# Optimization experiments

Measured on AMD Instinct MI355X. Metric: run time of the kernel, lower is better.

Reference implementation:

```python
import jax, jax.numpy as jnp
import numpy as np

H = 2048   # hidden_size
V = 50257  # output_size (vocab)


def setup_inputs() -> dict:
    key = jax.random.key(0)
    ks = jax.random.split(key, 8)
    s = 1.0 / np.sqrt(H)
    return {
        "word":   jax.random.normal(ks[0], (H,), dtype=jnp.float32),
        "hidden": jax.random.normal(ks[1], (1, 1, H), dtype=jnp.float32),
        "w_ih":   jax.random.uniform(ks[2], (3 * H, H), jnp.float32, -s, s),
        "w_hh":   jax.random.uniform(ks[3], (3 * H, H), jnp.float32, -s, s),
        "b_ih":   jax.random.uniform(ks[4], (3 * H,), jnp.float32, -s, s),
        "b_hh":   jax.random.uniform(ks[5], (3 * H,), jnp.float32, -s, s),
        "lin_w":  jax.random.uniform(ks[6], (V, H), jnp.float32, -s, s),
        "lin_b":  jax.random.uniform(ks[7], (V,), jnp.float32, -s, s),
    }


def reference(word, hidden, w_ih, w_hh, b_ih, b_hh, lin_w, lin_b):
    h0 = hidden.reshape(-1)                      # (H,)
    gi = w_ih @ word + b_ih                      # (3H,) input gates
    gh = w_hh @ h0 + b_hh                        # (3H,) hidden gates
    i_r, i_z, i_n = gi[:H], gi[H:2 * H], gi[2 * H:]
    h_r, h_z, h_n = gh[:H], gh[H:2 * H], gh[2 * H:]
    r = jax.nn.sigmoid(i_r + h_r)
    z = jax.nn.sigmoid(i_z + h_z)
    n = jnp.tanh(i_n + r * h_n)
    h_new = ((1.0 - z) * n + z * h0).reshape(1, 1, H)
    # NOTE: original computes probs from the OLD hidden, not h_new
    logits = hidden @ lin_w.T + lin_b            # (1,1,V)
    probs = jax.nn.softmax(logits, axis=-1)
    return (probs, h_new)
```

## Files before the change

### kernel.cpp

```cpp
#include <hip/hip_runtime.h>
#include <hip/hip_bf16.h>
#include <math.h>

#define H 2048
#define V 50257
#define KV4 (H / 4)
#define NBSM 128

typedef float f4 __attribute__((ext_vector_type(4)));

__device__ __forceinline__ f4 ntload(const f4* p) {
    return __builtin_nontemporal_load(p);
}

__device__ __forceinline__ float wave_reduce_sum(float x) {
    #pragma unroll
    for (int off = 32; off; off >>= 1) x += __shfl_down(x, off, 64);
    return x;
}

__device__ __forceinline__ float wave_allreduce_max(float x) {
    #pragma unroll
    for (int off = 32; off; off >>= 1) x = fmaxf(x, __shfl_xor(x, off, 64));
    return x;
}

__global__ __launch_bounds__(384) void gru_fused_kernel(
    const float* __restrict__ word, const float* __restrict__ h0,
    const float* __restrict__ w_ih, const float* __restrict__ w_hh,
    const float* __restrict__ b_ih, const float* __restrict__ b_hh,
    float* __restrict__ out_hnew) {
    __shared__ float red[6][4];
    const int lane = threadIdx.x & 63;
    const int w = threadIdx.x >> 6;
    const int j0 = blockIdx.x * 4;
    const int gate = (w < 3) ? w : (w - 3);
    const float* W = (w < 3) ? w_ih : w_hh;
    const f4* vec = reinterpret_cast<const f4*>((w < 3) ? word : h0);

    const size_t rb = (size_t)(gate * H + j0) * H;
    const f4* r0 = reinterpret_cast<const f4*>(W + rb);
    const f4* r1 = reinterpret_cast<const f4*>(W + rb + H);
    const f4* r2 = reinterpret_cast<const f4*>(W + rb + 2 * H);
    const f4* r3 = reinterpret_cast<const f4*>(W + rb + 3 * H);

    float a0 = 0.f, a1 = 0.f, a2 = 0.f, a3 = 0.f;
    #pragma unroll 4
    for (int k = lane; k < KV4; k += 64) {
        f4 x = vec[k];
        f4 p0 = ntload(&r0[k]);
        a0 += p0.x * x.x + p0.y * x.y + p0.z * x.z + p0.w * x.w;
        f4 p1 = ntload(&r1[k]);
        a1 += p1.x * x.x + p1.y * x.y + p1.z * x.z + p1.w * x.w;
        f4 p2 = ntload(&r2[k]);
        a2 += p2.x * x.x + p2.y * x.y + p2.z * x.z + p2.w * x.w;
        f4 p3 = ntload(&r3[k]);
        a3 += p3.x * x.x + p3.y * x.y + p3.z * x.z + p3.w * x.w;
    }
    a0 = wave_reduce_sum(a0);
    a1 = wave_reduce_sum(a1);
    a2 = wave_reduce_sum(a2);
    a3 = wave_reduce_sum(a3);
    if (lane == 0) {
        red[w][0] = a0; red[w][1] = a1; red[w][2] = a2; red[w][3] = a3;
    }
    __syncthreads();
    if (threadIdx.x < 4) {
        const int jj = threadIdx.x;
        const int j = j0 + jj;
        float ir = red[0][jj] + b_ih[j];
        float iz = red[1][jj] + b_ih[H + j];
        float in_ = red[2][jj] + b_ih[2 * H + j];
        float hr = red[3][jj] + b_hh[j];
        float hz = red[4][jj] + b_hh[H + j];
        float hn = red[5][jj] + b_hh[2 * H + j];
        float r = 1.f / (1.f + expf(-(ir + hr)));
        float z = 1.f / (1.f + expf(-(iz + hz)));
        float n = tanhf(in_ + r * hn);
        out_hnew[j] = (1.f - z) * n + z * h0[j];
    }
}

__global__ __launch_bounds__(256) void logits_kernel(
    const float* __restrict__ lin_w, const float* __restrict__ lin_b,
    const float* __restrict__ h0, float* __restrict__ logits) {
    const int lane = threadIdx.x & 63;
    const int wid = threadIdx.x >> 6;
    const int row0 = (blockIdx.x * 4 + wid) * 4;
    const int q0 = min(row0 + 0, V - 1);
    const int q1 = min(row0 + 1, V - 1);
    const int q2 = min(row0 + 2, V - 1);
    const int q3 = min(row0 + 3, V - 1);
    const f4* w0 = reinterpret_cast<const f4*>(lin_w + (size_t)q0 * H);
    const f4* w1 = reinterpret_cast<const f4*>(lin_w + (size_t)q1 * H);
    const f4* w2 = reinterpret_cast<const f4*>(lin_w + (size_t)q2 * H);
    const f4* w3 = reinterpret_cast<const f4*>(lin_w + (size_t)q3 * H);
    const f4* h4 = reinterpret_cast<const f4*>(h0);

    float a0 = 0.f, a1 = 0.f, a2 = 0.f, a3 = 0.f;
    #pragma unroll 4
    for (int k = lane; k < KV4; k += 64) {
        f4 h = h4[k];
        f4 p0 = ntload(&w0[k]);
        a0 += p0.x * h.x + p0.y * h.y + p0.z * h.z + p0.w * h.w;
        f4 p1 = ntload(&w1[k]);
        a1 += p1.x * h.x + p1.y * h.y + p1.z * h.z + p1.w * h.w;
        f4 p2 = ntload(&w2[k]);
        a2 += p2.x * h.x + p2.y * h.y + p2.z * h.z + p2.w * h.w;
        f4 p3 = ntload(&w3[k]);
        a3 += p3.x * h.x + p3.y * h.y + p3.z * h.z + p3.w * h.w;
    }
    a0 = wave_reduce_sum(a0);
    a1 = wave_reduce_sum(a1);
    a2 = wave_reduce_sum(a2);
    a3 = wave_reduce_sum(a3);
    if (lane == 0) {
        if (row0 + 0 < V) logits[row0 + 0] = a0 + lin_b[row0 + 0];
        if (row0 + 1 < V) logits[row0 + 1] = a1 + lin_b[row0 + 1];
        if (row0 + 2 < V) logits[row0 + 2] = a2 + lin_b[row0 + 2];
        if (row0 + 3 < V) logits[row0 + 3] = a3 + lin_b[row0 + 3];
    }
}

__global__ __launch_bounds__(256) void softmax_partial_kernel(
    const float* __restrict__ logits, float* __restrict__ pm,
    float* __restrict__ ps) {
    __shared__ float rm[4], rs[4];
    const int tid = threadIdx.x;
    const int lane = tid & 63;
    const int wid = tid >> 6;
    const int chunk = (V + NBSM - 1) / NBSM;
    const int start = blockIdx.x * chunk;
    const int end = min(V, start + chunk);

    float m = -INFINITY;
    for (int v = start + tid; v < end; v += 256) m = fmaxf(m, logits[v]);
    m = wave_allreduce_max(m);
    if (lane == 0) rm[wid] = m;
    __syncthreads();
    m = fmaxf(fmaxf(rm[0], rm[1]), fmaxf(rm[2], rm[3]));

    float s = 0.f;
    for (int v = start + tid; v < end; v += 256) s += expf(logits[v] - m);
    s = wave_reduce_sum(s);
    if (lane == 0) rs[wid] = s;
    __syncthreads();
    if (tid == 0) {
        pm[blockIdx.x] = m;
        ps[blockIdx.x] = rs[0] + rs[1] + rs[2] + rs[3];
    }
}

__global__ __launch_bounds__(256) void probs_kernel(
    const float* __restrict__ logits, const float* __restrict__ pm,
    const float* __restrict__ ps, float* __restrict__ out_probs) {
    __shared__ float sM, sInvS;
    if (threadIdx.x < 64) {
        const int lane = threadIdx.x;
        float m0 = pm[lane], s0 = ps[lane];
        float m1 = pm[lane + 64], s1 = ps[lane + 64];
        float M = fmaxf(m0, m1);
        float S = s0 * expf(m0 - M) + s1 * expf(m1 - M);
        #pragma unroll
        for (int off = 32; off; off >>= 1) {
            float Mo = __shfl_xor(M, off, 64);
            float So = __shfl_xor(S, off, 64);
            float Mn = fmaxf(M, Mo);
            S = S * expf(M - Mn) + So * expf(Mo - Mn);
            M = Mn;
        }
        if (lane == 0) { sM = M; sInvS = 1.f / S; }
    }
    __syncthreads();
    const int v = blockIdx.x * 256 + threadIdx.x;
    if (v < V) out_probs[v] = expf(logits[v] - sM) * sInvS;
}

extern "C" void kernel_launch(void* const* d_in, const int* in_sizes, int n_in,
                              void* d_out, int out_size, void* d_ws, size_t ws_size,
                              hipStream_t stream) {
    const float* word = (const float*)d_in[0];
    const float* hidden = (const float*)d_in[1];
    const float* w_ih = (const float*)d_in[2];
    const float* w_hh = (const float*)d_in[3];
    const float* b_ih = (const float*)d_in[4];
    const float* b_hh = (const float*)d_in[5];
    const float* lin_w = (const float*)d_in[6];
    const float* lin_b = (const float*)d_in[7];

    float* out = (float*)d_out;
    float* ws = (float*)d_ws;
    float* logits = ws;
    float* pm = ws + V + 64;
    float* ps = pm + NBSM;

    logits_kernel<<<(V + 15) / 16, 256, 0, stream>>>(lin_w, lin_b, hidden, logits);
    gru_fused_kernel<<<H / 4, 384, 0, stream>>>(word, hidden, w_ih, w_hh,
                                                b_ih, b_hh, out + V);
    softmax_partial_kernel<<<NBSM, 256, 0, stream>>>(logits, pm, ps);
    probs_kernel<<<(V + 255) / 256, 256, 0, stream>>>(logits, pm, ps, out);
}
```

Baseline: 103.9 us.

## Merge all matvecs into one grid with per-block softmax partials and finish kernel

Replaces four launches with two. A single matvec grid now covers the logits rows and both GRU gate matrices, and each logits block writes its own max and sum-exp partial. A finish kernel combines the 3142 partials and writes the probabilities, while one extra block applies the GRU gate math from the stored gate values. This removes the separate softmax partial pass over the logits and two launch boundaries, so the GRU weight stream can overlap the lin_w stream. In exchange, every finish block re-reduces thousands of partials and the gate values make an extra round trip through global memory.

Result: faster. 98.59 us (-5.1%).

```diff
diff --git a/kernel.cpp b/kernel.cpp
--- a/kernel.cpp
+++ b/kernel.cpp
@@ -5,7 +5,9 @@
 #define H 2048
 #define V 50257
 #define KV4 (H / 4)
-#define NBSM 128
+#define NB_LOG 3142
+#define NB_GRU 768
+#define NPART NB_LOG
 
 typedef float f4 __attribute__((ext_vector_type(4)));
 
@@ -19,161 +21,163 @@
     return x;
 }
 
-__device__ __forceinline__ float wave_allreduce_max(float x) {
-    #pragma unroll
-    for (int off = 32; off; off >>= 1) x = fmaxf(x, __shfl_xor(x, off, 64));
-    return x;
-}
-
-__global__ __launch_bounds__(384) void gru_fused_kernel(
+__global__ __launch_bounds__(256) void mega_matvec_kernel(
     const float* __restrict__ word, const float* __restrict__ h0,
     const float* __restrict__ w_ih, const float* __restrict__ w_hh,
     const float* __restrict__ b_ih, const float* __restrict__ b_hh,
-    float* __restrict__ out_hnew) {
-    __shared__ float red[6][4];
+    const float* __restrict__ lin_w, const float* __restrict__ lin_b,
+    float* __restrict__ gi, float* __restrict__ gh,
+    float* __restrict__ logits, float* __restrict__ pm,
+    float* __restrict__ ps) {
     const int lane = threadIdx.x & 63;
-    const int w = threadIdx.x >> 6;
-    const int j0 = blockIdx.x * 4;
-    const int gate = (w < 3) ? w : (w - 3);
-    const float* W = (w < 3) ? w_ih : w_hh;
-    const f4* vec = reinterpret_cast<const f4*>((w < 3) ? word : h0);
-
-    const size_t rb = (size_t)(gate * H + j0) * H;
-    const f4* r0 = reinterpret_cast<const f4*>(W + rb);
-    const f4* r1 = reinterpret_cast<const f4*>(W + rb + H);
-    const f4* r2 = reinterpret_cast<const f4*>(W + rb + 2 * H);
-    const f4* r3 = reinterpret_cast<const f4*>(W + rb + 3 * H);
+    const int wid = threadIdx.x >> 6;
+    __shared__ float lbuf[16];
+
+    const float* Wm;
+    const f4* vec;
+    const float* bias;
+    float* dst;
+    int r0, maxrow;
+    const bool is_log = ((int)blockIdx.x < NB_LOG);
+    if (is_log) {
+        Wm = lin_w; vec = reinterpret_cast<const f4*>(h0);
+        bias = lin_b; dst = logits;
+        r0 = blockIdx.x * 16 + wid * 4;
+        maxrow = V;
+    } else {
+        const int g = blockIdx.x - NB_LOG;
+        if (g < 384) {
+            Wm = w_ih; vec = reinterpret_cast<const f4*>(word);
+            bias = b_ih; dst = gi;
+            r0 = g * 16 + wid * 4;
+        } else {
+            Wm = w_hh; vec = reinterpret_cast<const f4*>(h0);
+            bias = b_hh; dst = gh;
+            r0 = (g - 384) * 16 + wid * 4;
+        }
+        maxrow = 3 * H;
+    }
+
+    const int q0 = min(r0 + 0, maxrow - 1);
+    const int q1 = min(r0 + 1, maxrow - 1);
+    const int q2 = min(r0 + 2, maxrow - 1);
+    const int q3 = min(r0 + 3, maxrow - 1);
+    const f4* w0 = reinterpret_cast<const f4*>(Wm + (size_t)q0 * H);
+    const f4* w1 = reinterpret_cast<const f4*>(Wm + (size_t)q1 * H);
+    const f4* w2 = reinterpret_cast<const f4*>(Wm + (size_t)q2 * H);
+    const f4* w3 = reinterpret_cast<const f4*>(Wm + (size_t)q3 * H);
 
     float a0 = 0.f, a1 = 0.f, a2 = 0.f, a3 = 0.f;
     #pragma unroll 4
     for (int k = lane; k < KV4; k += 64) {
         f4 x = vec[k];
-        f4 p0 = ntload(&r0[k]);
+        f4 p0 = ntload(&w0[k]);
         a0 += p0.x * x.x + p0.y * x.y + p0.z * x.z + p0.w * x.w;
-        f4 p1 = ntload(&r1[k]);
+        f4 p1 = ntload(&w1[k]);
         a1 += p1.x * x.x + p1.y * x.y + p1.z * x.z + p1.w * x.w;
-        f4 p2 = ntload(&r2[k]);
+        f4 p2 = ntload(&w2[k]);
         a2 += p2.x * x.x + p2.y * x.y + p2.z * x.z + p2.w * x.w;
-        f4 p3 = ntload(&r3[k]);
+        f4 p3 = ntload(&w3[k]);
         a3 += p3.x * x.x + p3.y * x.y + p3.z * x.z + p3.w * x.w;
     }
     a0 = wave_reduce_sum(a0);
     a1 = wave_reduce_sum(a1);
     a2 = wave_reduce_sum(a2);
     a3 = wave_reduce_sum(a3);
+
     if (lane == 0) {
-        red[w][0] = a0; red[w][1] = a1; red[w][2] = a2; red[w][3] = a3;
-    }
-    __syncthreads();
-    if (threadIdx.x < 4) {
-        const int jj = threadIdx.x;
-        const int j = j0 + jj;
-        float ir = red[0][jj] + b_ih[j];
-        float iz = red[1][jj] + b_ih[H + j];
-        float in_ = red[2][jj] + b_ih[2 * H + j];
-        float hr = red[3][jj] + b_hh[j];
-        float hz = red[4][jj] + b_hh[H + j];
-        float hn = red[5][jj] + b_hh[2 * H + j];
-        float r = 1.f / (1.f + expf(-(ir + hr)));
-        float z = 1.f / (1.f + expf(-(iz + hz)));
-        float n = tanhf(in_ + r * hn);
-        out_hnew[j] = (1.f - z) * n + z * h0[j];
-    }
-}
-
-__global__ __launch_bounds__(256) void logits_kernel(
-    const float* __restrict__ lin_w, const float* __restrict__ lin_b,
-    const float* __restrict__ h0, float* __restrict__ logits) {
-    const int lane = threadIdx.x & 63;
-    const int wid = threadIdx.x >> 6;
-    const int row0 = (blockIdx.x * 4 + wid) * 4;
-    const int q0 = min(row0 + 0, V - 1);
-    const int q1 = min(row0 + 1, V - 1);
-    const int q2 = min(row0 + 2, V - 1);
-    const int q3 = min(row0 + 3, V - 1);
-    const f4* w0 = reinterpret_cast<const f4*>(lin_w + (size_t)q0 * H);
-    const f4* w1 = reinterpret_cast<const f4*>(lin_w + (size_t)q1 * H);
-    const f4* w2 = reinterpret_cast<const f4*>(lin_w + (size_t)q2 * H);
-    const f4* w3 = reinterpret_cast<const f4*>(lin_w + (size_t)q3 * H);
-    const f4* h4 = reinterpret_cast<const f4*>(h0);
-
-    float a0 = 0.f, a1 = 0.f, a2 = 0.f, a3 = 0.f;
-    #pragma unroll 4
-    for (int k = lane; k < KV4; k += 64) {
-        f4 h = h4[k];
-        f4 p0 = ntload(&w0[k]);
-        a0 += p0.x * h.x + p0.y * h.y + p0.z * h.z + p0.w * h.w;
-        f4 p1 = ntload(&w1[k]);
-        a1 += p1.x * h.x + p1.y * h.y + p1.z * h.z + p1.w * h.w;
-        f4 p2 = ntload(&w2[k]);
-        a2 += p2.x * h.x + p2.y * h.y + p2.z * h.z + p2.w * h.w;
-        f4 p3 = ntload(&w3[k]);
-        a3 += p3.x * h.x + p3.y * h.y + p3.z * h.z + p3.w * h.w;
-    }
-    a0 = wave_reduce_sum(a0);
-    a1 = wave_reduce_sum(a1);
-    a2 = wave_reduce_sum(a2);
-    a3 = wave_reduce_sum(a3);
-    if (lane == 0) {
-        if (row0 + 0 < V) logits[row0 + 0] = a0 + lin_b[row0 + 0];
-        if (row0 + 1 < V) logits[row0 + 1] = a1 + lin_b[row0 + 1];
-        if (row0 + 2 < V) logits[row0 + 2] = a2 + lin_b[row0 + 2];
-        if (row0 + 3 < V) logits[row0 + 3] = a3 + lin_b[row0 + 3];
-    }
-}
-
-__global__ __launch_bounds__(256) void softmax_partial_kernel(
-    const float* __restrict__ logits, float* __restrict__ pm,
-    float* __restrict__ ps) {
-    __shared__ float rm[4], rs[4];
-    const int tid = threadIdx.x;
-    const int lane = tid & 63;
-    const int wid = tid >> 6;
-    const int chunk = (V + NBSM - 1) / NBSM;
-    const int start = blockIdx.x * chunk;
-    const int end = min(V, start + chunk);
-
-    float m = -INFINITY;
-    for (int v = start + tid; v < end; v += 256) m = fmaxf(m, logits[v]);
-    m = wave_allreduce_max(m);
-    if (lane == 0) rm[wid] = m;
-    __syncthreads();
-    m = fmaxf(fmaxf(rm[0], rm[1]), fmaxf(rm[2], rm[3]));
-
-    float s = 0.f;
-    for (int v = start + tid; v < end; v += 256) s += expf(logits[v] - m);
-    s = wave_reduce_sum(s);
-    if (lane == 0) rs[wid] = s;
-    __syncthreads();
-    if (tid == 0) {
-        pm[blockIdx.x] = m;
-        ps[blockIdx.x] = rs[0] + rs[1] + rs[2] + rs[3];
-    }
-}
-
-__global__ __launch_bounds__(256) void probs_kernel(
+        const float v0 = a0 + bias[q0];
+        const float v1 = a1 + bias[q1];
+        const float v2 = a2 + bias[q2];
+        const float v3 = a3 + bias[q3];
+        if (r0 + 0 < maxrow) dst[r0 + 0] = v0;
+        if (r0 + 1 < maxrow) dst[r0 + 1] = v1;
+        if (r0 + 2 < maxrow) dst[r0 + 2] = v2;
+        if (r0 + 3 < maxrow) dst[r0 + 3] = v3;
+        if (is_log) {
+            lbuf[wid * 4 + 0] = (r0 + 0 < maxrow) ? v0 : -INFINITY;
+            lbuf[wid * 4 + 1] = (r0 + 1 < maxrow) ? v1 : -INFINITY;
+            lbuf[wid * 4 + 2] = (r0 + 2 < maxrow) ? v2 : -INFINITY;
+            lbuf[wid * 4 + 3] = (r0 + 3 < maxrow) ? v3 : -INFINITY;
+        }
+    }
+    if (is_log) {
+        __syncthreads();
+        if (threadIdx.x < 16) {
+            const float x = lbuf[threadIdx.x];
+            float m = x;
+            #pragma unroll
+            for (int off = 8; off; off >>= 1)
+                m = fmaxf(m, __shfl_xor(m, off, 16));
+            float s = expf(x - m);
+            #pragma unroll
+            for (int off = 8; off; off >>= 1)
+                s += __shfl_xor(s, off, 16);
+            if (threadIdx.x == 0) {
+                pm[blockIdx.x] = m;
+                ps[blockIdx.x] = s;
+            }
+        }
+    }
+}
+
+__global__ __launch_bounds__(256) void finish_kernel(
     const float* __restrict__ logits, const float* __restrict__ pm,
-    const float* __restrict__ ps, float* __restrict__ out_probs) {
-    __shared__ float sM, sInvS;
-    if (threadIdx.x < 64) {
-        const int lane = threadIdx.x;
-        float m0 = pm[lane], s0 = ps[lane];
-        float m1 = pm[lane + 64], s1 = ps[lane + 64];
-        float M = fmaxf(m0, m1);
-        float S = s0 * expf(m0 - M) + s1 * expf(m1 - M);
+    const float* __restrict__ ps, const float* __restrict__ gi,
+    const float* __restrict__ gh, const float* __restrict__ h0,
+    float* __restrict__ out) {
+    if ((int)blockIdx.x < 50) {
+        __shared__ float redM[4], redS[4];
+        __shared__ float sM, sInvS;
+        const int lane = threadIdx.x & 63;
+        const int wid = threadIdx.x >> 6;
+
+        float M = -INFINITY, S = 0.f;
+        for (int p = threadIdx.x; p < NPART; p += 256) {
+            const float m = pm[p], s = ps[p];
+            const float Mn = fmaxf(M, m);
+            S = S * expf(M - Mn) + s * expf(m - Mn);
+            M = Mn;
+        }
         #pragma unroll
         for (int off = 32; off; off >>= 1) {
-            float Mo = __shfl_xor(M, off, 64);
-            float So = __shfl_xor(S, off, 64);
-            float Mn = fmaxf(M, Mo);
+            const float Mo = __shfl_xor(M, off, 64);
+            const float So = __shfl_xor(S, off, 64);
+            const float Mn = fmaxf(M, Mo);
             S = S * expf(M - Mn) + So * expf(Mo - Mn);
             M = Mn;
         }
-        if (lane == 0) { sM = M; sInvS = 1.f / S; }
-    }
-    __syncthreads();
-    const int v = blockIdx.x * 256 + threadIdx.x;
-    if (v < V) out_probs[v] = expf(logits[v] - sM) * sInvS;
+        if (lane == 0) { redM[wid] = M; redS[wid] = S; }
+        __syncthreads();
+        if (threadIdx.x == 0) {
+            float M4 = redM[0], S4 = redS[0];
+            #pragma unroll
+            for (int w = 1; w < 4; ++w) {
+                const float Mn = fmaxf(M4, redM[w]);
+                S4 = S4 * expf(M4 - Mn) + redS[w] * expf(redM[w] - Mn);
+                M4 = Mn;
+            }
+            sM = M4;
+            sInvS = 1.f / S4;
+        }
+        __syncthreads();
+        const float gm = sM, gis = sInvS;
+        const int base = blockIdx.x * 1024 + threadIdx.x;
+        #pragma unroll
+        for (int i = 0; i < 4; ++i) {
+            const int v = base + i * 256;
+            if (v < V) out[v] = expf(logits[v] - gm) * gis;
+        }
+    } else {
+        #pragma unroll
+        for (int i = 0; i < 8; ++i) {
+            const int j = threadIdx.x + i * 256;
+            const float r = 1.f / (1.f + expf(-(gi[j] + gh[j])));
+            const float z = 1.f / (1.f + expf(-(gi[H + j] + gh[H + j])));
+            const float n = tanhf(gi[2 * H + j] + r * gh[2 * H + j]);
+            out[V + j] = (1.f - z) * n + z * h0[j];
+        }
+    }
 }
 
 extern "C" void kernel_launch(void* const* d_in, const int* in_sizes, int n_in,
@@ -191,12 +195,13 @@
     float* out = (float*)d_out;
     float* ws = (float*)d_ws;
     float* logits = ws;
-    float* pm = ws + V + 64;
-    float* ps = pm + NBSM;
-
-    logits_kernel<<<(V + 15) / 16, 256, 0, stream>>>(lin_w, lin_b, hidden, logits);
-    gru_fused_kernel<<<H / 4, 384, 0, stream>>>(word, hidden, w_ih, w_hh,
-                                                b_ih, b_hh, out + V);
-    softmax_partial_kernel<<<NBSM, 256, 0, stream>>>(logits, pm, ps);
-    probs_kernel<<<(V + 255) / 256, 256, 0, stream>>>(logits, pm, ps, out);
-}
+    float* pm = ws + 50304;
+    float* ps = ws + 50304 + 3200;
+    float* gi = ws + 50304 + 6400;
+    float* gh = ws + 50304 + 6400 + 3 * H;
+
+    mega_matvec_kernel<<<NB_LOG + NB_GRU, 256, 0, stream>>>(
+        word, hidden, w_ih, w_hh, b_ih, b_hh, lin_w, lin_b,
+        gi, gh, logits, pm, ps);
+    finish_kernel<<<51, 256, 0, stream>>>(logits, pm, ps, gi, gh, hidden, out);
+}
```
